# Kernel tuning notes

Measured on AMD Instinct MI355X. Metric: run time of the kernel, lower is better.

## Reference

```python
import jax, jax.numpy as jnp
import numpy as np

N = 100000
E = 1600000
IN = 256
H = 4
D = 32      # n_hidden per head
C = 47      # n_classes
NEG_SLOPE = 0.2


def setup_inputs() -> dict:
    key = jax.random.key(0)
    ks = jax.random.split(key, 16)
    s = 0.1
    inp = {
        "x": jax.random.normal(ks[0], (N, IN), dtype=jnp.float32),
        "src": jax.random.randint(ks[1], (E,), 0, N),
        "dst": jax.random.randint(ks[2], (E,), 0, N),
        # layer 1: IN -> H*D
        "W1": jax.random.normal(ks[3], (IN, H * D), dtype=jnp.float32) * s,
        "al1": jax.random.normal(ks[4], (H, D), dtype=jnp.float32) * s,
        "ar1": jax.random.normal(ks[5], (H, D), dtype=jnp.float32) * s,
        "b1": jnp.zeros((H * D,), dtype=jnp.float32),
        # layer 2: H*D -> H*D
        "W2": jax.random.normal(ks[6], (H * D, H * D), dtype=jnp.float32) * s,
        "al2": jax.random.normal(ks[7], (H, D), dtype=jnp.float32) * s,
        "ar2": jax.random.normal(ks[8], (H, D), dtype=jnp.float32) * s,
        "b2": jnp.zeros((H * D,), dtype=jnp.float32),
        # layer 3: H*D -> H*C
        "W3": jax.random.normal(ks[9], (H * D, H * C), dtype=jnp.float32) * s,
        "al3": jax.random.normal(ks[10], (H, C), dtype=jnp.float32) * s,
        "ar3": jax.random.normal(ks[11], (H, C), dtype=jnp.float32) * s,
        "b3": jnp.zeros((H * C,), dtype=jnp.float32),
    }
    return inp


def gat_conv(h, W, al, ar, b, src, dst, out_dim, activate):
    # h: [N, F_in] -> feat: [N, H, out_dim]
    feat = (h @ W).reshape(N, H, out_dim)
    el = jnp.sum(feat * al[None], axis=-1)          # [N, H]
    er = jnp.sum(feat * ar[None], axis=-1)          # [N, H]
    e = jax.nn.leaky_relu(el[src] + er[dst], NEG_SLOPE)  # [E, H]
    # edge softmax per destination node (segment softmax)
    m = jax.ops.segment_max(e, dst, num_segments=N)      # [N, H]
    ex = jnp.exp(e - m[dst])                             # [E, H]
    den = jax.ops.segment_sum(ex, dst, num_segments=N)   # [N, H]
    alpha = ex / den[dst]                                # [E, H]
    # scatter-weighted aggregation: sum_e alpha_e * feat[src_e]
    out = jax.ops.segment_sum(feat[src] * alpha[:, :, None], dst, num_segments=N)
    out = out + b.reshape(1, H, out_dim)
    return jax.nn.relu(out) if activate else out


def reference(x, src, dst, W1, al1, ar1, b1, W2, al2, ar2, b2, W3, al3, ar3, b3):
    h = gat_conv(x, W1, al1, ar1, b1, src, dst, D, True).reshape(N, H * D)
    h = gat_conv(h, W2, al2, ar2, b2, src, dst, D, True).reshape(N, H * D)
    h = gat_conv(h, W3, al3, ar3, b3, src, dst, C, False)  # [N, H, C]
    h = h.mean(axis=1)                                     # head mean
    return jax.nn.log_softmax(h, axis=-1)
```

## Files before the change

kernel.cpp:

```cpp
#include <hip/hip_runtime.h>
#include <hip/hip_bf16.h>

typedef unsigned short ushort;
typedef unsigned int uint;
typedef __attribute__((ext_vector_type(8))) short short8;
typedef __attribute__((ext_vector_type(4))) float floatx4;
typedef __attribute__((ext_vector_type(2))) float floatx2;

#define NEG_SLOPE 0.2f

__device__ __forceinline__ float bu2f(ushort u) {
  uint t = ((uint)u) << 16;
  return __uint_as_float(t);
}
__device__ __forceinline__ ushort f2bu(float f) {
  __hip_bfloat16 h = __float2bfloat16(f);
  return *(ushort*)&h;
}
__device__ __forceinline__ float lo2f(uint u) { return __uint_as_float(u << 16); }
__device__ __forceinline__ float hi2f(uint u) { return __uint_as_float(u & 0xffff0000u); }
__device__ __forceinline__ float lrelu(float e) { return (e > 0.f) ? e : NEG_SLOPE * e; }
__device__ __forceinline__ float bperm(int byteaddr, float v) {
  return __uint_as_float((uint)__builtin_amdgcn_ds_bpermute(byteaddr, (int)__float_as_uint(v)));
}

__global__ void zero_int_kernel(int* __restrict__ p, int n) {
  int i = blockIdx.x * blockDim.x + threadIdx.x;
  if (i < n) p[i] = 0;
}

__global__ void hist_kernel(const int* __restrict__ dst, int* __restrict__ deg, int E) {
  int e = blockIdx.x * blockDim.x + threadIdx.x;
  if (e < E) atomicAdd(&deg[dst[e]], 1);
}

__global__ void scan1_kernel(const int* __restrict__ deg, int* __restrict__ part,
                             int* __restrict__ bsums, int n) {
  __shared__ int sdata[256];
  int t = threadIdx.x;
  int base = blockIdx.x * 1024;
  int v[4]; int s = 0;
#pragma unroll
  for (int j = 0; j < 4; ++j) {
    int idx = base + t * 4 + j;
    v[j] = (idx < n) ? deg[idx] : 0;
    s += v[j];
  }
  sdata[t] = s;
  __syncthreads();
  for (int off = 1; off < 256; off <<= 1) {
    int x = 0;
    if (t >= off) x = sdata[t - off];
    __syncthreads();
    if (t >= off) sdata[t] += x;
    __syncthreads();
  }
  if (t == 255) bsums[blockIdx.x] = sdata[255];
  int run = (t > 0) ? sdata[t - 1] : 0;
#pragma unroll
  for (int j = 0; j < 4; ++j) {
    int idx = base + t * 4 + j;
    if (idx < n) part[idx] = run;
    run += v[j];
  }
}

__global__ void scan2_kernel(int* __restrict__ bsums, int nb) {
  __shared__ int sdata[256];
  int t = threadIdx.x;
  sdata[t] = (t < nb) ? bsums[t] : 0;
  __syncthreads();
  for (int off = 1; off < 256; off <<= 1) {
    int x = 0;
    if (t >= off) x = sdata[t - off];
    __syncthreads();
    if (t >= off) sdata[t] += x;
    __syncthreads();
  }
  if (t < nb) bsums[t] = (t > 0) ? sdata[t - 1] : 0;
}

__global__ void scan3_kernel(const int* __restrict__ part, const int* __restrict__ bsums,
                             int* __restrict__ rowptr, int* __restrict__ cursor,
                             int n, int Etot) {
  int i = blockIdx.x * blockDim.x + threadIdx.x;
  if (i < n) {
    int v = part[i] + bsums[i >> 10];
    rowptr[i] = v;
    cursor[i] = v;
  }
  if (i == 0) rowptr[n] = Etot;
}

__global__ void scatter_kernel(const int* __restrict__ src, const int* __restrict__ dst,
                               int* __restrict__ cursor, int* __restrict__ csr_src, int E) {
  int e = blockIdx.x * blockDim.x + threadIdx.x;
  if (e < E) {
    int pos = atomicAdd(&cursor[dst[e]], 1);
    csr_src[pos] = src[e];
  }
}

__global__ void splitx_kernel(const float* __restrict__ x, ushort* __restrict__ xhi,
                              ushort* __restrict__ xlo, int n) {
  int base = (blockIdx.x * blockDim.x + threadIdx.x) * 4;
  if (base >= n) return;
  float4 a = *(const float4*)(x + base);
  float v[4] = {a.x, a.y, a.z, a.w};
  ushort hi[4], lo[4];
#pragma unroll
  for (int j = 0; j < 4; ++j) {
    hi[j] = f2bu(v[j]);
    lo[j] = f2bu(v[j] - bu2f(hi[j]));
  }
  uint2 ho, loo;
  ho.x = (uint)hi[0] | ((uint)hi[1] << 16);
  ho.y = (uint)hi[2] | ((uint)hi[3] << 16);
  loo.x = (uint)lo[0] | ((uint)lo[1] << 16);
  loo.y = (uint)lo[2] | ((uint)lo[3] << 16);
  *(uint2*)(xhi + base) = ho;
  *(uint2*)(xlo + base) = loo;
}

__global__ void splitW_kernel(const float* __restrict__ W, ushort* __restrict__ WtH,
                              ushort* __restrict__ WtL, int K, int Nc) {
  int idx = blockIdx.x * blockDim.x + threadIdx.x;
  if (idx >= K * Nc) return;
  int n = idx / K, k = idx - n * K;
  float w = W[(size_t)k * Nc + n];
  ushort hi = f2bu(w);
  WtH[idx] = hi;
  WtL[idx] = f2bu(w - bu2f(hi));
}

#define GBM 128
#define GBN 64
#define GBK 32
#define SA 40

__global__ __launch_bounds__(256) void gemm_split_kernel(
    const ushort* __restrict__ Ah, const ushort* __restrict__ Al,
    const ushort* __restrict__ Bh, const ushort* __restrict__ Bl,
    ushort* __restrict__ C, int M, int K, int Nc) {
  __shared__ ushort AsH[GBM * SA];
  __shared__ ushort AsL[GBM * SA];
  __shared__ ushort BsH[GBN * SA];
  __shared__ ushort BsL[GBN * SA];
  int tid = threadIdx.x;
  int lane = tid & 63;
  int wave = tid >> 6;
  int wm = wave & 1, wn = wave >> 1;
  int rowBase = blockIdx.y * GBM;
  int colBase = blockIdx.x * GBN;
  int q = lane >> 4;
  int ln = lane & 15;

  floatx4 acc[4][2] = {};

  for (int k0 = 0; k0 < K; k0 += GBK) {
#pragma unroll
    for (int it = 0; it < 2; ++it) {
      int i = tid + it * 256;
      int r = i >> 2, seg = i & 3;
      int grow = rowBase + r;
      uint4 vh = {0u, 0u, 0u, 0u}, vl = {0u, 0u, 0u, 0u};
      if (grow < M) {
        size_t off = (size_t)grow * K + k0 + seg * 8;
        vh = *(const uint4*)(Ah + off);
        vl = *(const uint4*)(Al + off);
      }
      *(uint4*)&AsH[r * SA + seg * 8] = vh;
      *(uint4*)&AsL[r * SA + seg * 8] = vl;
    }
    {
      int n = tid >> 2, seg = tid & 3;
      int gcol = colBase + n;
      uint4 vh = {0u, 0u, 0u, 0u}, vl = {0u, 0u, 0u, 0u};
      if (gcol < Nc) {
        size_t off = (size_t)gcol * K + k0 + seg * 8;
        vh = *(const uint4*)(Bh + off);
        vl = *(const uint4*)(Bl + off);
      }
      *(uint4*)&BsH[n * SA + seg * 8] = vh;
      *(uint4*)&BsL[n * SA + seg * 8] = vl;
    }
    __syncthreads();
    short8 afH[4], afL[4], bfH[2], bfL[2];
#pragma unroll
    for (int mt = 0; mt < 4; ++mt) {
      int r = (wm * 64 + mt * 16 + ln) * SA + q * 8;
      afH[mt] = *(const short8*)&AsH[r];
      afL[mt] = *(const short8*)&AsL[r];
    }
#pragma unroll
    for (int nt = 0; nt < 2; ++nt) {
      int r = (wn * 32 + nt * 16 + ln) * SA + q * 8;
      bfH[nt] = *(const short8*)&BsH[r];
      bfL[nt] = *(const short8*)&BsL[r];
    }
#pragma unroll
    for (int mt = 0; mt < 4; ++mt)
#pragma unroll
      for (int nt = 0; nt < 2; ++nt) {
        acc[mt][nt] = __builtin_amdgcn_mfma_f32_16x16x32_bf16(afH[mt], bfH[nt], acc[mt][nt], 0, 0, 0);
        acc[mt][nt] = __builtin_amdgcn_mfma_f32_16x16x32_bf16(afH[mt], bfL[nt], acc[mt][nt], 0, 0, 0);
        acc[mt][nt] = __builtin_amdgcn_mfma_f32_16x16x32_bf16(afL[mt], bfH[nt], acc[mt][nt], 0, 0, 0);
      }
    __syncthreads();
  }
#pragma unroll
  for (int mt = 0; mt < 4; ++mt) {
#pragma unroll
    for (int nt = 0; nt < 2; ++nt) {
      int col = colBase + wn * 32 + nt * 16 + ln;
      if (col < Nc) {
#pragma unroll
        for (int r = 0; r < 4; ++r) {
          int row = rowBase + wm * 64 + mt * 16 + q * 4 + r;
          if (row < M) C[(size_t)row * Nc + col] = f2bu(acc[mt][nt][r]);
        }
      }
    }
  }
}

__global__ void elr128_kernel(const ushort* __restrict__ feat, const float* __restrict__ al,
                              const float* __restrict__ ar, float* __restrict__ el,
                              float* __restrict__ er, int N) {
  int g = blockIdx.x * blockDim.x + threadIdx.x;
  if (g >= N * 4) return;
  int n = g >> 2, h = g & 3;
  const uint4* fp = (const uint4*)(feat + (size_t)n * 128 + h * 32);
  const float* alp = al + h * 32;
  const float* arp = ar + h * 32;
  float sl = 0.f, sr = 0.f;
#pragma unroll
  for (int b = 0; b < 4; ++b) {
    uint4 u = fp[b];
    uint w[4] = {u.x, u.y, u.z, u.w};
#pragma unroll
    for (int j = 0; j < 4; ++j) {
      int d = b * 8 + j * 2;
      float f0 = lo2f(w[j]), f1 = hi2f(w[j]);
      sl += f0 * alp[d] + f1 * alp[d + 1];
      sr += f0 * arp[d] + f1 * arp[d + 1];
    }
  }
  el[g] = sl;
  er[g] = sr;
}

__global__ void elr3_kernel(const ushort* __restrict__ feat, const float* __restrict__ al,
                            const float* __restrict__ ar, float* __restrict__ el,
                            float* __restrict__ er, int N) {
  int g = blockIdx.x * blockDim.x + threadIdx.x;
  if (g >= N * 4) return;
  int n = g >> 2, h = g & 3;
  const ushort* fp = feat + (size_t)n * 188 + h * 47;
  float sl = 0.f, sr = 0.f;
  for (int d = 0; d < 47; ++d) {
    float f = bu2f(fp[d]);
    sl += f * al[h * 47 + d];
    sr += f * ar[h * 47 + d];
  }
  el[g] = sl;
  er[g] = sr;
}

__global__ __launch_bounds__(256, 4) void agg128_kernel(
    const int* __restrict__ rowptr, const int* __restrict__ csr_src,
    const ushort* __restrict__ feat, const float* __restrict__ el,
    const float* __restrict__ er, const float* __restrict__ bias,
    ushort* __restrict__ hhi, ushort* __restrict__ hlo, int N) {
  int lane = threadIdx.x & 63;
  int v = blockIdx.x * 4 + (threadIdx.x >> 6);
  if (v >= N) return;
  float4 er4 = *(const float4*)(er + (size_t)v * 4);
  int r0 = rowptr[v], r1 = rowptr[v + 1];
  int hh = lane & 3;
  float eh = (hh == 0) ? er4.x : (hh == 1) ? er4.y : (hh == 2) ? er4.z : er4.w;
  int hf = lane >> 4;
  int hf4 = hf * 4;
  const uint* fb = (const uint*)feat;
  floatx2 c01 = {0.f, 0.f};
  float densum = 0.f;
  for (int i0 = r0; i0 < r1; i0 += 16) {
    int i = i0 + (lane >> 2);
    int sv = 0;
    float xv = 0.f;
    if (i < r1) {
      sv = csr_src[i];
      xv = __expf(lrelu(el[(size_t)sv * 4 + hh] + eh));
    }
    float ds = xv;
    ds += __shfl_xor(ds, 4);
    ds += __shfl_xor(ds, 8);
    ds += __shfl_xor(ds, 16);
    ds += __shfl_xor(ds, 32);
    densum += ds;
    int cnt = r1 - i0;
    if (cnt > 16) cnt = 16;
    if (cnt == 16) {
#pragma unroll
      for (int j = 0; j < 16; ++j) {
        int s = __builtin_amdgcn_readlane(sv, 4 * j);
        float x = bperm(16 * j + hf4, xv);
        uint u = fb[((size_t)(uint)s << 6) + lane];
        floatx2 f = {lo2f(u), hi2f(u)};
        floatx2 xx = {x, x};
        c01 += xx * f;
      }
    } else {
      for (int j = 0; j < cnt; ++j) {
        int s = __builtin_amdgcn_readlane(sv, 4 * j);
        float x = __shfl(xv, 4 * j + hf);
        uint u = fb[((size_t)(uint)s << 6) + lane];
        floatx2 f = {lo2f(u), hi2f(u)};
        floatx2 xx = {x, x};
        c01 += xx * f;
      }
    }
  }
  float den = __shfl(densum, hf);
  float o0 = (den > 0.f) ? c01.x / den : 0.f;
  float o1 = (den > 0.f) ? c01.y / den : 0.f;
  o0 = fmaxf(o0 + bias[2 * lane], 0.f);
  o1 = fmaxf(o1 + bias[2 * lane + 1], 0.f);
  ushort h0 = f2bu(o0), h1 = f2bu(o1);
  ushort l0 = f2bu(o0 - bu2f(h0)), l1 = f2bu(o1 - bu2f(h1));
  ((uint*)hhi)[(size_t)v * 64 + lane] = (uint)h0 | ((uint)h1 << 16);
  ((uint*)hlo)[(size_t)v * 64 + lane] = (uint)l0 | ((uint)l1 << 16);
}

__global__ __launch_bounds__(256) void agg3_kernel(
    const int* __restrict__ rowptr, const int* __restrict__ csr_src,
    const ushort* __restrict__ feat, const float* __restrict__ el,
    const float* __restrict__ er, const float* __restrict__ bias,
    float* __restrict__ out, int N) {
  __shared__ float svm[4][188];
  int lane = threadIdx.x & 63;
  int w = threadIdx.x >> 6;
  int v = blockIdx.x * 4 + w;
  bool valid = (v < N);
  float4 er4 = {0.f, 0.f, 0.f, 0.f};
  int r0 = 0, r1 = 0;
  if (valid) {
    er4 = *(const float4*)(er + (size_t)v * 4);
    r0 = rowptr[v];
    r1 = rowptr[v + 1];
  }
  int hh = lane & 3;
  float eh = (hh == 0) ? er4.x : (hh == 1) ? er4.y : (hh == 2) ? er4.z : er4.w;
  int fa = 2 * lane, fbi = 2 * lane + 1;
  int fc = 128 + 2 * lane, fd = 129 + 2 * lane;
  bool hasC = (fd < 188);
  int ha = fa / 47, hb = fbi / 47;
  int hc = hasC ? fc / 47 : 3, hd = hasC ? fd / 47 : 3;
  const uint* fpb = (const uint*)feat;
  float aa = 0.f, ab = 0.f, ac = 0.f, ad = 0.f;
  float da = 0.f, db = 0.f, dc = 0.f, dd = 0.f;
  for (int i0 = r0; i0 < r1; i0 += 16) {
    int i = i0 + (lane >> 2);
    int sv = 0;
    float xv = 0.f;
    if (i < r1) {
      sv = csr_src[i];
      xv = __expf(lrelu(el[(size_t)sv * 4 + hh] + eh));
    }
    int cnt = r1 - i0;
    if (cnt > 16) cnt = 16;
#pragma unroll 2
    for (int j = 0; j < cnt; ++j) {
      int s = __builtin_amdgcn_readlane(sv, j * 4);
      float xa = __shfl(xv, j * 4 + ha);
      float xb = __shfl(xv, j * 4 + hb);
      const uint* fr = fpb + (size_t)(uint)s * 94;
      uint u0 = fr[lane];
      da += xa; db += xb;
      aa += xa * lo2f(u0);
      ab += xb * hi2f(u0);
      if (hasC) {
        float xc = __shfl(xv, j * 4 + hc);
        float xd = __shfl(xv, j * 4 + hd);
        uint u1 = fr[64 + lane];
        dc += xc; dd += xd;
        ac += xc * lo2f(u1);
        ad += xd * hi2f(u1);
      }
    }
  }
  float oa = ((da > 0.f) ? aa / da : 0.f) + bias[fa];
  float ob = ((db > 0.f) ? ab / db : 0.f) + bias[fbi];
  if (valid) {
    svm[w][fa] = oa;
    svm[w][fbi] = ob;
    if (hasC) {
      float oc = ((dc > 0.f) ? ac / dc : 0.f) + bias[fc];
      float od = ((dd > 0.f) ? ad / dd : 0.f) + bias[fd];
      svm[w][fc] = oc;
      svm[w][fd] = od;
    }
  }
  __syncthreads();
  float val = -1e30f;
  if (valid && lane < 47)
    val = 0.25f * (svm[w][lane] + svm[w][47 + lane] + svm[w][94 + lane] + svm[w][141 + lane]);
  float mx = val;
#pragma unroll
  for (int off = 32; off > 0; off >>= 1) mx = fmaxf(mx, __shfl_xor(mx, off));
  float ex = (lane < 47) ? __expf(val - mx) : 0.f;
  float sum = ex;
#pragma unroll
  for (int off = 32; off > 0; off >>= 1) sum += __shfl_xor(sum, off);
  float res = val - mx - logf(sum);
  if (valid && lane < 47) out[(size_t)v * 47 + lane] = res;
}

extern "C" void kernel_launch(void* const* d_in, const int* in_sizes, int n_in,
                              void* d_out, int out_size, void* d_ws, size_t ws_size,
                              hipStream_t stream) {
  const int N = 100000, E = 1600000, IN = 256;
  const int F = 128;
  const int F3 = 188;

  const float* x = (const float*)d_in[0];
  const int* src = (const int*)d_in[1];
  const int* dst = (const int*)d_in[2];
  const float* W1 = (const float*)d_in[3];
  const float* al1 = (const float*)d_in[4];
  const float* ar1 = (const float*)d_in[5];
  const float* b1 = (const float*)d_in[6];
  const float* W2 = (const float*)d_in[7];
  const float* al2 = (const float*)d_in[8];
  const float* ar2 = (const float*)d_in[9];
  const float* b2 = (const float*)d_in[10];
  const float* W3 = (const float*)d_in[11];
  const float* al3 = (const float*)d_in[12];
  const float* ar3 = (const float*)d_in[13];
  const float* b3 = (const float*)d_in[14];

  char* p = (char*)d_ws;
  auto alloc = [&](size_t bytes) -> char* {
    char* r = p;
    p += (bytes + 255) & ~(size_t)255;
    return r;
  };
  ushort* xhi = (ushort*)alloc((size_t)N * IN * sizeof(ushort));
  ushort* xlo = (ushort*)alloc((size_t)N * IN * sizeof(ushort));
  ushort* feat = (ushort*)alloc((size_t)N * F3 * sizeof(ushort));
  ushort* Wt1h = (ushort*)alloc((size_t)F * IN * sizeof(ushort));
  ushort* Wt1l = (ushort*)alloc((size_t)F * IN * sizeof(ushort));
  ushort* Wt2h = (ushort*)alloc((size_t)F * F * sizeof(ushort));
  ushort* Wt2l = (ushort*)alloc((size_t)F * F * sizeof(ushort));
  ushort* Wt3h = (ushort*)alloc((size_t)F3 * F * sizeof(ushort));
  ushort* Wt3l = (ushort*)alloc((size_t)F3 * F * sizeof(ushort));
  float* el = (float*)alloc((size_t)N * 4 * sizeof(float));
  float* er = (float*)alloc((size_t)N * 4 * sizeof(float));
  int* deg = (int*)alloc((size_t)N * sizeof(int));
  int* part = (int*)alloc((size_t)N * sizeof(int));
  int* bsums = (int*)alloc(256 * sizeof(int));
  int* rowptr = (int*)alloc((size_t)(N + 1) * sizeof(int));
  int* cursor = (int*)alloc((size_t)N * sizeof(int));
  int* csr_src = (int*)alloc((size_t)E * sizeof(int));

  ushort* hhi = xhi;
  ushort* hlo = xlo;

  zero_int_kernel<<<(N + 255) / 256, 256, 0, stream>>>(deg, N);
  hist_kernel<<<(E + 255) / 256, 256, 0, stream>>>(dst, deg, E);
  int nb = (N + 1023) / 1024;
  scan1_kernel<<<nb, 256, 0, stream>>>(deg, part, bsums, N);
  scan2_kernel<<<1, 256, 0, stream>>>(bsums, nb);
  scan3_kernel<<<(N + 255) / 256, 256, 0, stream>>>(part, bsums, rowptr, cursor, N, E);
  scatter_kernel<<<(E + 255) / 256, 256, 0, stream>>>(src, dst, cursor, csr_src, E);

  splitx_kernel<<<(N * IN / 4 + 255) / 256, 256, 0, stream>>>(x, xhi, xlo, N * IN);
  splitW_kernel<<<(IN * F + 255) / 256, 256, 0, stream>>>(W1, Wt1h, Wt1l, IN, F);
  splitW_kernel<<<(F * F + 255) / 256, 256, 0, stream>>>(W2, Wt2h, Wt2l, F, F);
  splitW_kernel<<<(F * F3 + 255) / 256, 256, 0, stream>>>(W3, Wt3h, Wt3l, F, F3);

  int rowBlocks = (N + GBM - 1) / GBM;
  int nodeBlocks = (N + 3) / 4;

  gemm_split_kernel<<<dim3(F / GBN, rowBlocks), 256, 0, stream>>>(
      xhi, xlo, Wt1h, Wt1l, feat, N, IN, F);
  elr128_kernel<<<(N * 4 + 255) / 256, 256, 0, stream>>>(feat, al1, ar1, el, er, N);
  agg128_kernel<<<nodeBlocks, 256, 0, stream>>>(rowptr, csr_src, feat, el, er, b1, hhi, hlo, N);

  gemm_split_kernel<<<dim3(F / GBN, rowBlocks), 256, 0, stream>>>(
      hhi, hlo, Wt2h, Wt2l, feat, N, F, F);
  elr128_kernel<<<(N * 4 + 255) / 256, 256, 0, stream>>>(feat, al2, ar2, el, er, N);
  agg128_kernel<<<nodeBlocks, 256, 0, stream>>>(rowptr, csr_src, feat, el, er, b2, hhi, hlo, N);

  gemm_split_kernel<<<dim3((F3 + GBN - 1) / GBN, rowBlocks), 256, 0, stream>>>(
      hhi, hlo, Wt3h, Wt3l, feat, N, F, F3);
  elr3_kernel<<<(N * 4 + 255) / 256, 256, 0, stream>>>(feat, al3, ar3, el, er, N);
  agg3_kernel<<<nodeBlocks, 256, 0, stream>>>(rowptr, csr_src, feat, el, er, b3,
                                              (float*)d_out, N);
}
```

Measured before the change: 926.1 us.

## Drop low-bf16 split of activations in GEMMs and streamline agg3 denominators

Activations are now kept only as a single bf16 copy, so the split-bf16 GEMM uses two MFMAs per tile instead of three. It also stops reading and writing the low-part activation arrays in splitx, the GEMMs and agg128. In agg3, the four per-head denominator sums are replaced by one cross-lane reduction per chunk, and the hasC branch becomes unconditional loads using an offset. This trades activation precision for less memory traffic and MFMA work, at some risk to accuracy.

Result: faster. 850.1 us (-8.2%).

```diff
diff --git a/kernel.cpp b/kernel.cpp
--- a/kernel.cpp
+++ b/kernel.cpp
@@ -101,25 +101,18 @@
   }
 }
 
-__global__ void splitx_kernel(const float* __restrict__ x, ushort* __restrict__ xhi,
-                              ushort* __restrict__ xlo, int n) {
+__global__ void splitx_kernel(const float* __restrict__ x, ushort* __restrict__ xhi, int n) {
   int base = (blockIdx.x * blockDim.x + threadIdx.x) * 4;
   if (base >= n) return;
   float4 a = *(const float4*)(x + base);
   float v[4] = {a.x, a.y, a.z, a.w};
-  ushort hi[4], lo[4];
-#pragma unroll
-  for (int j = 0; j < 4; ++j) {
-    hi[j] = f2bu(v[j]);
-    lo[j] = f2bu(v[j] - bu2f(hi[j]));
-  }
-  uint2 ho, loo;
+  ushort hi[4];
+#pragma unroll
+  for (int j = 0; j < 4; ++j) hi[j] = f2bu(v[j]);
+  uint2 ho;
   ho.x = (uint)hi[0] | ((uint)hi[1] << 16);
   ho.y = (uint)hi[2] | ((uint)hi[3] << 16);
-  loo.x = (uint)lo[0] | ((uint)lo[1] << 16);
-  loo.y = (uint)lo[2] | ((uint)lo[3] << 16);
   *(uint2*)(xhi + base) = ho;
-  *(uint2*)(xlo + base) = loo;
 }
 
 __global__ void splitW_kernel(const float* __restrict__ W, ushort* __restrict__ WtH,
@@ -139,11 +132,10 @@
 #define SA 40
 
 __global__ __launch_bounds__(256) void gemm_split_kernel(
-    const ushort* __restrict__ Ah, const ushort* __restrict__ Al,
+    const ushort* __restrict__ A,
     const ushort* __restrict__ Bh, const ushort* __restrict__ Bl,
     ushort* __restrict__ C, int M, int K, int Nc) {
-  __shared__ ushort AsH[GBM * SA];
-  __shared__ ushort AsL[GBM * SA];
+  __shared__ ushort As[GBM * SA];
   __shared__ ushort BsH[GBN * SA];
   __shared__ ushort BsL[GBN * SA];
   int tid = threadIdx.x;
@@ -163,14 +155,12 @@
       int i = tid + it * 256;
       int r = i >> 2, seg = i & 3;
       int grow = rowBase + r;
-      uint4 vh = {0u, 0u, 0u, 0u}, vl = {0u, 0u, 0u, 0u};
+      uint4 vh = {0u, 0u, 0u, 0u};
       if (grow < M) {
         size_t off = (size_t)grow * K + k0 + seg * 8;
-        vh = *(const uint4*)(Ah + off);
-        vl = *(const uint4*)(Al + off);
-      }
-      *(uint4*)&AsH[r * SA + seg * 8] = vh;
-      *(uint4*)&AsL[r * SA + seg * 8] = vl;
+        vh = *(const uint4*)(A + off);
+      }
+      *(uint4*)&As[r * SA + seg * 8] = vh;
     }
     {
       int n = tid >> 2, seg = tid & 3;
@@ -185,12 +175,11 @@
       *(uint4*)&BsL[n * SA + seg * 8] = vl;
     }
     __syncthreads();
-    short8 afH[4], afL[4], bfH[2], bfL[2];
+    short8 af[4], bfH[2], bfL[2];
 #pragma unroll
     for (int mt = 0; mt < 4; ++mt) {
       int r = (wm * 64 + mt * 16 + ln) * SA + q * 8;
-      afH[mt] = *(const short8*)&AsH[r];
-      afL[mt] = *(const short8*)&AsL[r];
+      af[mt] = *(const short8*)&As[r];
     }
 #pragma unroll
     for (int nt = 0; nt < 2; ++nt) {
@@ -202,9 +191,8 @@
     for (int mt = 0; mt < 4; ++mt)
 #pragma unroll
       for (int nt = 0; nt < 2; ++nt) {
-        acc[mt][nt] = __builtin_amdgcn_mfma_f32_16x16x32_bf16(afH[mt], bfH[nt], acc[mt][nt], 0, 0, 0);
-        acc[mt][nt] = __builtin_amdgcn_mfma_f32_16x16x32_bf16(afH[mt], bfL[nt], acc[mt][nt], 0, 0, 0);
-        acc[mt][nt] = __builtin_amdgcn_mfma_f32_16x16x32_bf16(afL[mt], bfH[nt], acc[mt][nt], 0, 0, 0);
+        acc[mt][nt] = __builtin_amdgcn_mfma_f32_16x16x32_bf16(af[mt], bfH[nt], acc[mt][nt], 0, 0, 0);
+        acc[mt][nt] = __builtin_amdgcn_mfma_f32_16x16x32_bf16(af[mt], bfL[nt], acc[mt][nt], 0, 0, 0);
       }
     __syncthreads();
   }
@@ -271,7 +259,7 @@
     const int* __restrict__ rowptr, const int* __restrict__ csr_src,
     const ushort* __restrict__ feat, const float* __restrict__ el,
     const float* __restrict__ er, const float* __restrict__ bias,
-    ushort* __restrict__ hhi, ushort* __restrict__ hlo, int N) {
+    ushort* __restrict__ hhi, int N) {
   int lane = threadIdx.x & 63;
   int v = blockIdx.x * 4 + (threadIdx.x >> 6);
   if (v >= N) return;
@@ -327,9 +315,7 @@
   o0 = fmaxf(o0 + bias[2 * lane], 0.f);
   o1 = fmaxf(o1 + bias[2 * lane + 1], 0.f);
   ushort h0 = f2bu(o0), h1 = f2bu(o1);
-  ushort l0 = f2bu(o0 - bu2f(h0)), l1 = f2bu(o1 - bu2f(h1));
   ((uint*)hhi)[(size_t)v * 64 + lane] = (uint)h0 | ((uint)h1 << 16);
-  ((uint*)hlo)[(size_t)v * 64 + lane] = (uint)l0 | ((uint)l1 << 16);
 }
 
 __global__ __launch_bounds__(256) void agg3_kernel(
@@ -356,9 +342,10 @@
   bool hasC = (fd < 188);
   int ha = fa / 47, hb = fbi / 47;
   int hc = hasC ? fc / 47 : 3, hd = hasC ? fd / 47 : 3;
+  int off2 = hasC ? 64 : 0;
   const uint* fpb = (const uint*)feat;
   float aa = 0.f, ab = 0.f, ac = 0.f, ad = 0.f;
-  float da = 0.f, db = 0.f, dc = 0.f, dd = 0.f;
+  float densum = 0.f;
   for (int i0 = r0; i0 < r1; i0 += 16) {
     int i = i0 + (lane >> 2);
     int sv = 0;
@@ -367,6 +354,12 @@
       sv = csr_src[i];
       xv = __expf(lrelu(el[(size_t)sv * 4 + hh] + eh));
     }
+    float ds = xv;
+    ds += __shfl_xor(ds, 4);
+    ds += __shfl_xor(ds, 8);
+    ds += __shfl_xor(ds, 16);
+    ds += __shfl_xor(ds, 32);
+    densum += ds;
     int cnt = r1 - i0;
     if (cnt > 16) cnt = 16;
 #pragma unroll 2
@@ -374,21 +367,21 @@
       int s = __builtin_amdgcn_readlane(sv, j * 4);
       float xa = __shfl(xv, j * 4 + ha);
       float xb = __shfl(xv, j * 4 + hb);
+      float xc = __shfl(xv, j * 4 + hc);
+      float xd = __shfl(xv, j * 4 + hd);
       const uint* fr = fpb + (size_t)(uint)s * 94;
       uint u0 = fr[lane];
-      da += xa; db += xb;
-      aa += xa * lo2f(u0);
-      ab += xb * hi2f(u0);
-      if (hasC) {
-        float xc = __shfl(xv, j * 4 + hc);
-        float xd = __shfl(xv, j * 4 + hd);
-        uint u1 = fr[64 + lane];
-        dc += xc; dd += xd;
-        ac += xc * lo2f(u1);
-        ad += xd * hi2f(u1);
-      }
-    }
-  }
+      uint u1 = fr[off2 + lane];
+      aa = fmaf(xa, lo2f(u0), aa);
+      ab = fmaf(xb, hi2f(u0), ab);
+      ac = fmaf(xc, lo2f(u1), ac);
+      ad = fmaf(xd, hi2f(u1), ad);
+    }
+  }
+  float da = __shfl(densum, ha);
+  float db = __shfl(densum, hb);
+  float dc = __shfl(densum, hc);
+  float dd = __shfl(densum, hd);
   float oa = ((da > 0.f) ? aa / da : 0.f) + bias[fa];
   float ob = ((db > 0.f) ? ab / db : 0.f) + bias[fbi];
   if (valid) {
@@ -446,7 +439,6 @@
     return r;
   };
   ushort* xhi = (ushort*)alloc((size_t)N * IN * sizeof(ushort));
-  ushort* xlo = (ushort*)alloc((size_t)N * IN * sizeof(ushort));
   ushort* feat = (ushort*)alloc((size_t)N * F3 * sizeof(ushort));
   ushort* Wt1h = (ushort*)alloc((size_t)F * IN * sizeof(ushort));
   ushort* Wt1l = (ushort*)alloc((size_t)F * IN * sizeof(ushort));
@@ -464,7 +456,6 @@
   int* csr_src = (int*)alloc((size_t)E * sizeof(int));
 
   ushort* hhi = xhi;
-  ushort* hlo = xlo;
 
   zero_int_kernel<<<(N + 255) / 256, 256, 0, stream>>>(deg, N);
   hist_kernel<<<(E + 255) / 256, 256, 0, stream>>>(dst, deg, E);
@@ -474,7 +465,7 @@
   scan3_kernel<<<(N + 255) / 256, 256, 0, stream>>>(part, bsums, rowptr, cursor, N, E);
   scatter_kernel<<<(E + 255) / 256, 256, 0, stream>>>(src, dst, cursor, csr_src, E);
 
-  splitx_kernel<<<(N * IN / 4 + 255) / 256, 256, 0, stream>>>(x, xhi, xlo, N * IN);
+  splitx_kernel<<<(N * IN / 4 + 255) / 256, 256, 0, stream>>>(x, xhi, N * IN);
   splitW_kernel<<<(IN * F + 255) / 256, 256, 0, stream>>>(W1, Wt1h, Wt1l, IN, F);
   splitW_kernel<<<(F * F + 255) / 256, 256, 0, stream>>>(W2, Wt2h, Wt2l, F, F);
   splitW_kernel<<<(F * F3 + 255) / 256, 256, 0, stream>>>(W3, Wt3h, Wt3l, F, F3);
@@ -483,17 +474,17 @@
   int nodeBlocks = (N + 3) / 4;
 
   gemm_split_kernel<<<dim3(F / GBN, rowBlocks), 256, 0, stream>>>(
-      xhi, xlo, Wt1h, Wt1l, feat, N, IN, F);
+      xhi, Wt1h, Wt1l, feat, N, IN, F);
   elr128_kernel<<<(N * 4 + 255) / 256, 256, 0, stream>>>(feat, al1, ar1, el, er, N);
-  agg128_kernel<<<nodeBlocks, 256, 0, stream>>>(rowptr, csr_src, feat, el, er, b1, hhi, hlo, N);
+  agg128_kernel<<<nodeBlocks, 256, 0, stream>>>(rowptr, csr_src, feat, el, er, b1, hhi, N);
 
   gemm_split_kernel<<<dim3(F / GBN, rowBlocks), 256, 0, stream>>>(
-      hhi, hlo, Wt2h, Wt2l, feat, N, F, F);
+      hhi, Wt2h, Wt2l, feat, N, F, F);
   elr128_kernel<<<(N * 4 + 255) / 256, 256, 0, stream>>>(feat, al2, ar2, el, er, N);
-  agg128_kernel<<<nodeBlocks, 256, 0, stream>>>(rowptr, csr_src, feat, el, er, b2, hhi, hlo, N);
+  agg128_kernel<<<nodeBlocks, 256, 0, stream>>>(rowptr, csr_src, feat, el, er, b2, hhi, N);
 
   gemm_split_kernel<<<dim3((F3 + GBN - 1) / GBN, rowBlocks), 256, 0, stream>>>(
-      hhi, hlo, Wt3h, Wt3l, feat, N, F, F3);
+      hhi, Wt3h, Wt3l, feat, N, F, F3);
   elr3_kernel<<<(N * 4 + 255) / 256, 256, 0, stream>>>(feat, al3, ar3, el, er, N);
   agg3_kernel<<<nodeBlocks, 256, 0, stream>>>(rowptr, csr_src, feat, el, er, b3,
                                               (float*)d_out, N);
```
